# Optimization experiments

Hardware: AMD Instinct MI355X
Metric: run time of the kernel (lower is better)

Reference implementation:

```python
import jax, jax.numpy as jnp
import numpy as np

DN = ('NCHW', 'OIHW', 'NCHW')


def conv2d(x, w, pad, dil):
    return jax.lax.conv_general_dilated(x, w, (1, 1), [(pad, pad), (pad, pad)],
                                        rhs_dilation=(dil, dil), dimension_numbers=DN)


def group_norm(x, scale, bias, groups=16, eps=1e-5):
    B, C, H, W = x.shape
    xg = x.reshape(B, groups, -1)
    mu = xg.mean(-1, keepdims=True)
    var = xg.var(-1, keepdims=True)
    xg = (xg - mu) / jnp.sqrt(var + eps)
    return xg.reshape(B, C, H, W) * scale[None, :, None, None] + bias[None, :, None, None]


def aspp_block(x, w, s, b, pad, dil):
    return jax.nn.relu(group_norm(conv2d(x, w, pad, dil), s, b))


def cc_module(q, k, v):
    # criss-cross attention with channel-cosine-normalized q/k
    eps = 1e-10
    qn = q / (jnp.sqrt(jnp.sum(q * q, axis=1, keepdims=True)) + eps)  # norm over channel
    kn = k / (jnp.sqrt(jnp.sum(k * k, axis=1, keepdims=True)) + eps)
    H = q.shape[2]
    # energy along column (vary h') and row (vary w')
    eH = jnp.einsum('bchw,bcgw->bhwg', qn, kn)  # [B,H,W,H]
    eW = jnp.einsum('bchw,bchv->bhwv', qn, kn)  # [B,H,W,W]
    att = jax.nn.softmax(jnp.concatenate([eH, eW], axis=-1), axis=-1)
    attH, attW = att[..., :H], att[..., H:]
    outH = jnp.einsum('bcgw,bhwg->bchw', v, attH)
    outW = jnp.einsum('bchv,bhwv->bchw', v, attW)
    return outH + outW


def cam_module(x, gamma):
    # channel attention with spatial-cosine-normalized similarity
    B, C, H, W = x.shape
    f = x.reshape(B, C, H * W)
    fn = f / (jnp.sqrt(jnp.sum(f * f, axis=-1, keepdims=True)) + 1e-10)
    energy = jnp.einsum('bcn,bdn->bcd', fn, fn)  # [B,C,C]
    att = jax.nn.softmax(energy, axis=-1)
    out = jnp.einsum('bcd,bdn->bcn', att, f).reshape(B, C, H, W)
    return gamma * out + x


def setup_inputs() -> dict:
    key = jax.random.key(0)
    ks = jax.random.split(key, 32)
    C, Cq = 256, 64
    d = {}
    d['x'] = jax.random.normal(ks[0], (4, C, 128, 128), dtype=jnp.float32)
    d['w1'] = jax.random.normal(ks[1], (C, C, 1, 1), jnp.float32) * 0.05
    d['w2'] = jax.random.normal(ks[2], (C, C, 3, 3), jnp.float32) * 0.02
    d['w3'] = jax.random.normal(ks[3], (C, C, 3, 3), jnp.float32) * 0.02
    d['w4'] = jax.random.normal(ks[4], (C, C, 3, 3), jnp.float32) * 0.02
    d['wc'] = jax.random.normal(ks[5], (C, C, 3, 3), jnp.float32) * 0.02
    for i, nm in enumerate(['s1', 's2', 's3', 's4', 'sc']):
        d[nm] = jnp.ones((C,), jnp.float32)
    for nm in ['b1', 'b2', 'b3', 'b4', 'bc']:
        d[nm] = jnp.zeros((C,), jnp.float32)
    d['wq'] = jax.random.normal(ks[6], (Cq, C, 1, 1), jnp.float32) * 0.05
    d['bq'] = jnp.zeros((Cq,), jnp.float32)
    d['wk'] = jax.random.normal(ks[7], (Cq, C, 1, 1), jnp.float32) * 0.05
    d['bk'] = jnp.zeros((Cq,), jnp.float32)
    d['wv'] = jax.random.normal(ks[8], (C, C, 1, 1), jnp.float32) * 0.05
    d['bv'] = jnp.zeros((C,), jnp.float32)
    d['gammas'] = jax.random.normal(ks[9], (5,), jnp.float32) * 0.1
    return d


def reference(x, w1, w2, w3, w4, wc, s1, s2, s3, s4, sc, b1, b2, b3, b4, bc,
              wq, bq, wk, bk, wv, bv, gammas):
    dil = (1, 6, 12, 18)
    x1 = aspp_block(x, w1, s1, b1, pad=0, dil=dil[0])
    x2 = aspp_block(x, w2, s2, b2, pad=dil[1], dil=dil[1])
    x3 = aspp_block(x, w3, s3, b3, pad=dil[2], dil=dil[2])
    x4 = aspp_block(x, w4, s4, b4, pad=dil[3], dil=dil[3])
    x5 = aspp_block(x, wc, sc, bc, pad=1, dil=1)
    for _ in range(2):
        q = conv2d(x5, wq, 0, 1) + bq[None, :, None, None]
        k = conv2d(x5, wk, 0, 1) + bk[None, :, None, None]
        v = conv2d(x5, wv, 0, 1) + bv[None, :, None, None]
        x5 = cc_module(q, k, v)
    L = [x1, x2, x3, x4, x5]
    L = [cam_module(L[i], gammas[i]) for i in range(5)]
    return jnp.stack(L)  # [5, B, C, H, W]
```

## Files before the change

kernel.cpp:

```cpp
#include <hip/hip_runtime.h>
#include <hip/hip_bf16.h>

typedef __hip_bfloat16 bf16;
typedef unsigned short u16;
typedef __attribute__((ext_vector_type(8))) short short8v;
typedef __attribute__((ext_vector_type(4))) float f32x4;

#define BB   4
#define CC_  256
#define HH   128
#define WW   128
#define HWn  16384
#define SZ   ((size_t)16777216)

__device__ __forceinline__ float b2f(bf16 v){ return __bfloat162float(v); }
__device__ __forceinline__ bf16  f2b(float v){ return __float2bfloat16(v); }
__device__ __forceinline__ float us2f(u16 u){
  union { unsigned int i; float f; } x; x.i = ((unsigned int)u) << 16; return x.f;
}
__device__ __forceinline__ u16 f2us(float v){
  bf16 h = f2b(v); u16 u; __builtin_memcpy(&u, &h, 2); return u;
}
__device__ __forceinline__ void st4(float* p, float a, float b, float c, float d){
  *(float4*)p = make_float4(a,b,c,d);
}
__device__ __forceinline__ void st4(bf16* p, float a, float b, float c, float d){
  bf16 o[4] = { f2b(a), f2b(b), f2b(c), f2b(d) };
  *(uint2*)p = *(uint2*)o;
}
__device__ __forceinline__ void store1(float* p, float v){ *p = v; }
__device__ __forceinline__ void store1(bf16* p, float v){ *p = f2b(v); }

typedef __attribute__((address_space(1))) const unsigned int u32g;
typedef __attribute__((address_space(3))) unsigned int u32l;
__device__ __forceinline__ void gl16(const void* g, void* l)
{
  u32g* gp = (u32g*)(unsigned long long)(size_t)g;
  u32l* lp = (u32l*)(unsigned int)(size_t)l;
  __builtin_amdgcn_global_load_lds(gp, lp, 16, 0, 0);
}

__global__ __launch_bounds__(256)
void k_xpose(const float* __restrict__ x, bf16* __restrict__ xt)
{
  const int b = blockIdx.x >> 7, h = blockIdx.x & 127;
  __shared__ u16 L[64][132];
  const int tid = threadIdx.x;
  for (int c0 = 0; c0 < 256; c0 += 64) {
    for (int idx = tid; idx < 2048; idx += 256) {
      const int c = idx >> 5, w4 = (idx & 31) * 4;
      const float4 v = *(const float4*)&x[(((size_t)(b*CC_ + c0 + c))*HH + h)*WW + w4];
      L[c][w4]   = f2us(v.x); L[c][w4+1] = f2us(v.y);
      L[c][w4+2] = f2us(v.z); L[c][w4+3] = f2us(v.w);
    }
    __syncthreads();
    for (int idx = tid; idx < 1024; idx += 256) {
      const int w = idx >> 3, cg = (idx & 7) * 8;
      u16 tmp[8];
      #pragma unroll
      for (int j = 0; j < 8; ++j) tmp[j] = L[cg + j][w];
      *(uint4*)&xt[(((size_t)(b*HH + h))*WW + w)*256 + c0 + cg] = *(uint4*)tmp;
    }
    __syncthreads();
  }
}

__global__ __launch_bounds__(256)
void k_xposeb_b(const bf16* __restrict__ xt, bf16* __restrict__ fb)
{
  const int b = blockIdx.x >> 7, h = blockIdx.x & 127;
  __shared__ u16 L[64][132];
  const int tid = threadIdx.x;
  for (int c0 = 0; c0 < 256; c0 += 64) {
    for (int idx = tid; idx < 1024; idx += 256) {
      const int w = idx >> 3, cg = (idx & 7) * 8;
      u16 t[8];
      *(uint4*)t = *(const uint4*)((const u16*)xt + (((size_t)(b*HH + h))*WW + w)*256 + c0 + cg);
      #pragma unroll
      for (int j = 0; j < 8; ++j) L[cg + j][w] = t[j];
    }
    __syncthreads();
    for (int idx = tid; idx < 2048; idx += 256) {
      const int c = idx >> 5, w4 = (idx & 31) * 4;
      u16 q[4] = { L[c][w4], L[c][w4+1], L[c][w4+2], L[c][w4+3] };
      *(uint2*)((u16*)fb + (((size_t)(b*CC_ + c0 + c))*HH + h)*WW + w4) = *(uint2*)q;
    }
    __syncthreads();
  }
}

__global__ __launch_bounds__(256)
void k_wt(const float* __restrict__ w, bf16* __restrict__ wt, int taps)
{
  const int i = blockIdx.x * 256 + threadIdx.x;
  const int tap = i >> 16, r = i & 65535;
  const int co = r >> 8, ci = r & 255;
  if (tap < taps) wt[i] = f2b(w[(co*256 + ci)*taps + tap]);
}

template<int KHW, typename DT, bool TRANS, bool STATS>
__global__ __launch_bounds__(256)
void k_convm(const bf16* __restrict__ xt, const bf16* __restrict__ wt,
             const float* __restrict__ bias, DT* __restrict__ dst, int dil, int CO,
             float* __restrict__ stats)
{
  const int b   = blockIdx.y >> 7;
  const int h   = blockIdx.y & 127;
  const int co0 = blockIdx.x * 64;
  const int tid = threadIdx.x;
  const int wid = tid >> 6;
  const int lane = tid & 63;
  const int lr = lane & 15;
  const int lg = lane >> 4;
  const int lrow = lane >> 2;
  const int lci  = (lane & 3) * 8;

  __shared__ __align__(16) u16 Asld[KHW*64][32];
  __shared__ __align__(16) u16 Bsld[164][32];

  for (int i = tid; i < 36*32; i += 256) {
    int r = i >> 5; r = (r < 18) ? r : (128 + r);
    Bsld[r][i & 31] = 0;
  }

  f32x4 acc[4][2] = {};

  for (int kh = 0; kh < KHW; ++kh) {
    const int hh = h + (kh - (KHW >> 1)) * dil;
    if (hh < 0 || hh >= HH) continue;
    const bf16* __restrict__ brow = xt + ((size_t)(b*HH + hh))*WW*256;
    for (int kc = 0; kc < 256; kc += 32) {
      for (int ch = wid; ch < KHW*4; ch += 4) {
        const int row = ch*16 + lrow;
        const int tap = row >> 6, cc = row & 63;
        gl16(wt + ((size_t)(kh*KHW + tap))*CO*256 + (co0 + cc)*256 + kc + lci,
             &Asld[ch*16][0]);
      }
      for (int ch = wid; ch < 8; ch += 4) {
        const int wpos = ch*16 + lrow;
        gl16(brow + (size_t)wpos*256 + kc + lci, &Bsld[18 + ch*16][0]);
      }
      __syncthreads();
      #pragma unroll
      for (int kw = 0; kw < KHW; ++kw) {
        const int pbase = 18 + (kw - (KHW >> 1)) * dil;
        short8v af[4], bfr[2];
        #pragma unroll
        for (int cf = 0; cf < 4; ++cf)
          af[cf] = *(const short8v*)&Asld[kw*64 + cf*16 + lr][lg*8];
        #pragma unroll
        for (int wf = 0; wf < 2; ++wf)
          bfr[wf] = *(const short8v*)&Bsld[pbase + wid*32 + wf*16 + lr][lg*8];
        #pragma unroll
        for (int cf = 0; cf < 4; ++cf)
          #pragma unroll
          for (int wf = 0; wf < 2; ++wf)
            acc[cf][wf] = __builtin_amdgcn_mfma_f32_16x16x32_bf16(
                            af[cf], bfr[wf], acc[cf][wf], 0, 0, 0);
      }
      __syncthreads();
    }
  }
  if constexpr (TRANS) {
    #pragma unroll
    for (int cf = 0; cf < 4; ++cf) {
      float bb[4];
      #pragma unroll
      for (int r = 0; r < 4; ++r)
        bb[r] = bias ? bias[co0 + cf*16 + lg*4 + r] : 0.f;
      #pragma unroll
      for (int wf = 0; wf < 2; ++wf) {
        const int wpix = wid*32 + wf*16 + lr;
        bf16* dr = (bf16*)dst + (((size_t)(b*HH + h))*WW + wpix)*CO + co0 + cf*16 + lg*4;
        bf16 o4[4];
        #pragma unroll
        for (int r = 0; r < 4; ++r) o4[r] = f2b(acc[cf][wf][r] + bb[r]);
        *(uint2*)dr = *(uint2*)o4;
      }
    }
  } else {
    float s0[4] = {0.f,0.f,0.f,0.f}, s1[4] = {0.f,0.f,0.f,0.f};
    #pragma unroll
    for (int cf = 0; cf < 4; ++cf) {
      #pragma unroll
      for (int r = 0; r < 4; ++r) {
        const int co = co0 + cf*16 + lg*4 + r;
        const float bb = bias ? bias[co] : 0.f;
        DT* drow = dst + (((size_t)(b*CO + co))*HH + h)*WW;
        #pragma unroll
        for (int wf = 0; wf < 2; ++wf) {
          const float v = acc[cf][wf][r] + bb;
          store1(drow + wid*32 + wf*16 + lr, v);
          if constexpr (STATS) {
            const float vr = us2f(f2us(v));
            s0[cf] += vr;
            s1[cf] = fmaf(vr, vr, s1[cf]);
          }
        }
      }
    }
    if constexpr (STATS) {
      #pragma unroll
      for (int cf = 0; cf < 4; ++cf)
        #pragma unroll
        for (int o = 32; o > 0; o >>= 1) {
          s0[cf] += __shfl_down(s0[cf], o, 64);
          s1[cf] += __shfl_down(s1[cf], o, 64);
        }
      __shared__ float sred[4][4][2];
      if (lane == 0) {
        #pragma unroll
        for (int cf = 0; cf < 4; ++cf) { sred[wid][cf][0] = s0[cf]; sred[wid][cf][1] = s1[cf]; }
      }
      __syncthreads();
      if (tid < 8) {
        const int cf = tid >> 1, j = tid & 1;
        const float t = sred[0][cf][j] + sred[1][cf][j] + sred[2][cf][j] + sred[3][cf][j];
        atomicAdd(&stats[(b*16 + (co0 >> 4) + cf)*2 + j], t);
      }
    }
  }
}

__global__ __launch_bounds__(256)
void k_gn_apply16(const bf16* __restrict__ t, const float* __restrict__ stats,
                  const float* __restrict__ sc, const float* __restrict__ bi,
                  float* __restrict__ dst)
{
  const size_t e = ((size_t)blockIdx.x * 256 + threadIdx.x) * 4;
  const int c  = (int)((e >> 14) & 255);
  const int bg = (int)(e >> 22) * 16 + (c >> 4);
  const float cnt = 16.f * 16384.f;
  const float mu  = stats[bg*2] / cnt;
  const float var = stats[bg*2+1] / cnt - mu * mu;
  const float rs  = rsqrtf(var + 1e-5f);
  const float a   = rs * sc[c];
  const float bb  = bi[c] - mu * a;
  const ushort4 u = *(const ushort4*)((const u16*)t + e);
  st4(dst + e, fmaxf(us2f(u.x)*a+bb,0.f), fmaxf(us2f(u.y)*a+bb,0.f),
               fmaxf(us2f(u.z)*a+bb,0.f), fmaxf(us2f(u.w)*a+bb,0.f));
}

__global__ __launch_bounds__(256)
void k_gn_applyb(const bf16* __restrict__ t, const float* __restrict__ stats,
                 const float* __restrict__ sc, const float* __restrict__ bi,
                 bf16* __restrict__ dst, float* __restrict__ rownsq)
{
  const size_t e = ((size_t)blockIdx.x * 256 + threadIdx.x) * 4;
  const int c  = (int)((e >> 14) & 255);
  const int bg = (int)(e >> 22) * 16 + (c >> 4);
  const float cnt = 16.f * 16384.f;
  const float mu  = stats[bg*2] / cnt;
  const float var = stats[bg*2+1] / cnt - mu * mu;
  const float rs  = rsqrtf(var + 1e-5f);
  const float a   = rs * sc[c];
  const float bb  = bi[c] - mu * a;
  const ushort4 u = *(const ushort4*)((const u16*)t + e);
  u16 q[4] = { f2us(fmaxf(us2f(u.x)*a+bb,0.f)), f2us(fmaxf(us2f(u.y)*a+bb,0.f)),
               f2us(fmaxf(us2f(u.z)*a+bb,0.f)), f2us(fmaxf(us2f(u.w)*a+bb,0.f)) };
  *(uint2*)((u16*)dst + e) = *(uint2*)q;
  float sq = 0.f;
  #pragma unroll
  for (int j = 0; j < 4; ++j) { const float w = us2f(q[j]); sq = fmaf(w, w, sq); }
  #pragma unroll
  for (int o = 32; o > 0; o >>= 1) sq += __shfl_down(sq, o, 64);
  __shared__ float sh[4];
  const int wid = threadIdx.x >> 6, lane = threadIdx.x & 63;
  if (lane == 0) sh[wid] = sq;
  __syncthreads();
  if (threadIdx.x == 0) atomicAdd(&rownsq[blockIdx.x >> 4], sh[0]+sh[1]+sh[2]+sh[3]);
}

__global__ __launch_bounds__(256)
void k_energym(const bf16* __restrict__ fb, float* __restrict__ energy)
{
  const int b  = blockIdx.z;
  const int c0 = (blockIdx.x >> 1) * 128, d0 = (blockIdx.x & 1) * 128;
  const int k0 = blockIdx.y * 512;
  __shared__ __align__(16) u16 Au[2][128][32];
  __shared__ __align__(16) u16 Bu[2][128][32];
  const int tid = threadIdx.x;
  const int wid = tid >> 6, lane = tid & 63;
  const int lr = lane & 15, lg = lane >> 4;
  const int lrow = lane >> 2, lci = (lane & 3) * 8;
  const int row0w = (wid & 1) * 64, col0w = (wid >> 1) * 64;
  const u16* __restrict__ fbb = (const u16*)fb + (size_t)b * CC_ * HWn;

  f32x4 acc[4][4] = {};

  for (int kc = 0; kc < 512; kc += 64) {
    for (int ci = wid; ci < 16; ci += 4) {
      const int seg = ci >> 3, rq = (ci & 7) * 16;
      const int m = rq + lrow;
      gl16(fbb + (size_t)(c0 + m)*HWn + k0 + kc + seg*32 + lci, &Au[seg][rq][0]);
      gl16(fbb + (size_t)(d0 + m)*HWn + k0 + kc + seg*32 + lci, &Bu[seg][rq][0]);
    }
    __syncthreads();
    #pragma unroll
    for (int ks = 0; ks < 2; ++ks) {
      short8v af[4], bfv[4];
      #pragma unroll
      for (int cf = 0; cf < 4; ++cf)
        af[cf] = *(const short8v*)&Au[ks][row0w + cf*16 + lr][lg*8];
      #pragma unroll
      for (int df = 0; df < 4; ++df)
        bfv[df] = *(const short8v*)&Bu[ks][col0w + df*16 + lr][lg*8];
      #pragma unroll
      for (int cf = 0; cf < 4; ++cf)
        #pragma unroll
        for (int df = 0; df < 4; ++df)
          acc[cf][df] = __builtin_amdgcn_mfma_f32_16x16x32_bf16(
                          af[cf], bfv[df], acc[cf][df], 0, 0, 0);
    }
    __syncthreads();
  }
  #pragma unroll
  for (int cf = 0; cf < 4; ++cf)
    #pragma unroll
    for (int df = 0; df < 4; ++df)
      #pragma unroll
      for (int r = 0; r < 4; ++r) {
        const int row = c0 + row0w + cf*16 + lg*4 + r;
        const int col = d0 + col0w + df*16 + lr;
        atomicAdd(&energy[((size_t)(b*CC_ + row))*CC_ + col], acc[cf][df][r]);
      }
}

__global__ __launch_bounds__(512)
void k_camoutm(const float* __restrict__ catt, const bf16* __restrict__ fb,
               float* __restrict__ fio, const float* __restrict__ gammas, int gi)
{
  const int b  = blockIdx.y;
  const int n0 = blockIdx.x * 128;
  __shared__ u16 Au[256][40];
  __shared__ u16 Bu[128][40];
  const int tid = threadIdx.x;
  const int wid = tid >> 6, lane = tid & 63;
  const int lr = lane & 15, lg = lane >> 4;
  const int row0w = (wid & 3) * 64, col0w = (wid >> 2) * 64;

  f32x4 acc[4][4] = {};

  for (int k0 = 0; k0 < 256; k0 += 32) {
    {
      const int m = tid >> 1, kh = (tid & 1) * 16;
      const float* src = catt + ((size_t)(b*CC_ + m))*CC_ + k0 + kh;
      u16 t[16];
      #pragma unroll
      for (int j = 0; j < 4; ++j) {
        const float4 v = *(const float4*)(src + j*4);
        t[j*4]=f2us(v.x); t[j*4+1]=f2us(v.y); t[j*4+2]=f2us(v.z); t[j*4+3]=f2us(v.w);
      }
      *(uint4*)&Au[m][kh]   = *(uint4*)&t[0];
      *(uint4*)&Au[m][kh+8] = *(uint4*)&t[8];
    }
    {
      const int kk = tid >> 4, cl = tid & 15;
      const u16* src = (const u16*)fb + ((size_t)(b*CC_ + k0 + kk))*HWn + n0 + cl;
      #pragma unroll
      for (int j = 0; j < 8; ++j)
        Bu[cl + 16*j][kk] = src[16*j];
    }
    __syncthreads();
    short8v af[4], bfv[4];
    #pragma unroll
    for (int cf = 0; cf < 4; ++cf)
      af[cf] = *(const short8v*)&Au[row0w + cf*16 + lr][lg*8];
    #pragma unroll
    for (int df = 0; df < 4; ++df)
      bfv[df] = *(const short8v*)&Bu[col0w + df*16 + lr][lg*8];
    #pragma unroll
    for (int cf = 0; cf < 4; ++cf)
      #pragma unroll
      for (int df = 0; df < 4; ++df)
        acc[cf][df] = __builtin_amdgcn_mfma_f32_16x16x32_bf16(
                        af[cf], bfv[df], acc[cf][df], 0, 0, 0);
    __syncthreads();
  }
  const float g = gammas[gi];
  #pragma unroll
  for (int cf = 0; cf < 4; ++cf)
    #pragma unroll
    for (int df = 0; df < 4; ++df)
      #pragma unroll
      for (int r = 0; r < 4; ++r) {
        const int row = row0w + cf*16 + lg*4 + r;
        const int col = n0 + col0w + df*16 + lr;
        const size_t o = ((size_t)(b*CC_ + row))*HWn + col;
        fio[o] = g*acc[cf][df][r] + us2f(((const u16*)fb)[o]);
      }
}

__global__ __launch_bounds__(256)
void k_qknorm_t(bf16* __restrict__ q)
{
  const int pix = blockIdx.x * 256 + threadIdx.x;
  u16* __restrict__ base = (u16*)q + (size_t)pix * 64;
  u16 t[64];
  #pragma unroll
  for (int j = 0; j < 8; ++j) *(uint4*)&t[j*8] = *(const uint4*)(base + j*8);
  float s = 0.f;
  #pragma unroll
  for (int c = 0; c < 64; ++c) { const float v = us2f(t[c]); s = fmaf(v, v, s); }
  const float rn = 1.f / (sqrtf(s) + 1e-10f);
  #pragma unroll
  for (int c = 0; c < 64; ++c) t[c] = f2us(us2f(t[c]) * rn);
  #pragma unroll
  for (int j = 0; j < 8; ++j) *(uint4*)(base + j*8) = *(uint4*)&t[j*8];
}

__global__ __launch_bounds__(256)
void k_attHm(const bf16* __restrict__ qt, const bf16* __restrict__ kt,
             bf16* __restrict__ att)
{
  const int b = blockIdx.x >> 7, w = blockIdx.x & 127;
  __shared__ __align__(16) u16 Qs[2][128][32];
  __shared__ __align__(16) u16 Ks[2][128][32];
  const int tid = threadIdx.x;
  const int wid = tid >> 6, lane = tid & 63;
  const int lr = lane & 15, lg = lane >> 4;
  const int lrow = lane >> 2, lci = (lane & 3) * 8;
  const int h0w = (wid & 1) * 64, g0w = (wid >> 1) * 64;
  for (int ci = wid; ci < 16; ci += 4) {
    const int seg = ci >> 3, rq = (ci & 7) * 16;
    const int row = rq + lrow;
    const size_t gb = (((size_t)(b*HH + row))*WW + w)*64 + seg*32 + lci;
    gl16((const u16*)qt + gb, &Qs[seg][rq][0]);
    gl16((const u16*)kt + gb, &Ks[seg][rq][0]);
  }
  __syncthreads();
  f32x4 acc[4][4] = {};
  #pragma unroll
  for (int ks = 0; ks < 2; ++ks) {
    short8v af[4], bfv[4];
    #pragma unroll
    for (int hf = 0; hf < 4; ++hf)
      af[hf] = *(const short8v*)&Qs[ks][h0w + hf*16 + lr][lg*8];
    #pragma unroll
    for (int gf = 0; gf < 4; ++gf)
      bfv[gf] = *(const short8v*)&Ks[ks][g0w + gf*16 + lr][lg*8];
    #pragma unroll
    for (int hf = 0; hf < 4; ++hf)
      #pragma unroll
      for (int gf = 0; gf < 4; ++gf)
        acc[hf][gf] = __builtin_amdgcn_mfma_f32_16x16x32_bf16(
                        af[hf], bfv[gf], acc[hf][gf], 0, 0, 0);
  }
  #pragma unroll
  for (int hf = 0; hf < 4; ++hf)
    #pragma unroll
    for (int r = 0; r < 4; ++r) {
      const int h = h0w + hf*16 + lg*4 + r;
      u16* prow = (u16*)att + (((size_t)b*HH + h)*WW + w)*256 + g0w;
      #pragma unroll
      for (int gf = 0; gf < 4; ++gf)
        prow[gf*16 + lr] = f2us(acc[hf][gf][r]);
    }
}

__global__ __launch_bounds__(256)
void k_attWm(const bf16* __restrict__ qt, const bf16* __restrict__ kt,
             bf16* __restrict__ att)
{
  const int b = blockIdx.x >> 7, h = blockIdx.x & 127;
  __shared__ __align__(16) u16 Qs[2][128][32];
  __shared__ __align__(16) u16 Ks[2][128][32];
  const int tid = threadIdx.x;
  const int wid = tid >> 6, lane = tid & 63;
  const int lr = lane & 15, lg = lane >> 4;
  const int lrow = lane >> 2, lci = (lane & 3) * 8;
  const int w0w = (wid & 1) * 64, v0w = (wid >> 1) * 64;
  for (int ci = wid; ci < 16; ci += 4) {
    const int seg = ci >> 3, rq = (ci & 7) * 16;
    const int row = rq + lrow;
    const size_t gb = (((size_t)(b*HH + h))*WW + row)*64 + seg*32 + lci;
    gl16((const u16*)qt + gb, &Qs[seg][rq][0]);
    gl16((const u16*)kt + gb, &Ks[seg][rq][0]);
  }
  __syncthreads();
  f32x4 acc[4][4] = {};
  #pragma unroll
  for (int ks = 0; ks < 2; ++ks) {
    short8v af[4], bfv[4];
    #pragma unroll
    for (int wf = 0; wf < 4; ++wf)
      af[wf] = *(const short8v*)&Qs[ks][w0w + wf*16 + lr][lg*8];
    #pragma unroll
    for (int vf = 0; vf < 4; ++vf)
      bfv[vf] = *(const short8v*)&Ks[ks][v0w + vf*16 + lr][lg*8];
    #pragma unroll
    for (int wf = 0; wf < 4; ++wf)
      #pragma unroll
      for (int vf = 0; vf < 4; ++vf)
        acc[wf][vf] = __builtin_amdgcn_mfma_f32_16x16x32_bf16(
                        af[wf], bfv[vf], acc[wf][vf], 0, 0, 0);
  }
  #pragma unroll
  for (int wf = 0; wf < 4; ++wf)
    #pragma unroll
    for (int r = 0; r < 4; ++r) {
      const int wloc = w0w + wf*16 + lg*4 + r;
      u16* prow = (u16*)att + ((((size_t)b*HH + h)*WW + wloc)*256 + 128) + v0w;
      #pragma unroll
      for (int vf = 0; vf < 4; ++vf)
        prow[vf*16 + lr] = f2us(acc[wf][vf][r]);
    }
}

__global__ __launch_bounds__(256)
void k_ccsm(bf16* __restrict__ att)
{
  const int row  = blockIdx.x * 4 + (threadIdx.x >> 6);
  const int lane = threadIdx.x & 63;
  u16* __restrict__ p = (u16*)att + (size_t)row * 256 + lane * 4;
  const ushort4 u = *(const ushort4*)p;
  float v0 = us2f(u.x), v1 = us2f(u.y), v2 = us2f(u.z), v3 = us2f(u.w);
  float m = fmaxf(fmaxf(v0, v1), fmaxf(v2, v3));
  #pragma unroll
  for (int o = 32; o; o >>= 1) m = fmaxf(m, __shfl_xor(m, o, 64));
  const float e0 = __expf(v0-m), e1 = __expf(v1-m), e2 = __expf(v2-m), e3 = __expf(v3-m);
  float s = e0 + e1 + e2 + e3;
  #pragma unroll
  for (int o = 32; o; o >>= 1) s += __shfl_xor(s, o, 64);
  const float inv = 1.f / s;
  st4((bf16*)p, e0*inv, e1*inv, e2*inv, e3*inv);
}

__global__ __launch_bounds__(256)
void k_outWm(const bf16* __restrict__ vt, const bf16* __restrict__ att,
             bf16* __restrict__ yt)
{
  const int b = blockIdx.y >> 7, h = blockIdx.y & 127;
  const int ch0 = blockIdx.x * 128;
  __shared__ u16 As[128][72];
  __shared__ u16 Bs[128][72];
  const int tid = threadIdx.x;
  const int wid = tid >> 6, lane = tid & 63;
  const int lr = lane & 15, lg = lane >> 4;
  const int w0w = (wid & 1) * 64, c0w = (wid >> 1) * 64;

  f32x4 acc[4][4] = {};

  for (int v0 = 0; v0 < 128; v0 += 64) {
    {
      const int row = tid >> 1, kq = (tid & 1) * 32;
      const u16* src = (const u16*)att + ((((size_t)b*HH + h)*WW + row)*256 + 128) + v0 + kq;
      #pragma unroll
      for (int j = 0; j < 4; ++j)
        *(uint4*)&As[row][kq + j*8] = *(const uint4*)(src + j*8);
    }
    {
      const int vv = tid & 63, cg0 = (tid >> 6) * 32;
      #pragma unroll
      for (int j2 = 0; j2 < 4; ++j2) {
        const int c8 = cg0 + j2*8;
        u16 t[8];
        *(uint4*)t = *(const uint4*)((const u16*)vt +
            (((size_t)(b*HH + h))*WW + (v0 + vv))*256 + ch0 + c8);
        #pragma unroll
        for (int jj = 0; jj < 8; ++jj) Bs[c8 + jj][vv] = t[jj];
      }
    }
    __syncthreads();
    #pragma unroll
    for (int ks = 0; ks < 2; ++ks) {
      short8v af[4], bfv[4];
      #pragma unroll
      for (int wf = 0; wf < 4; ++wf)
        af[wf] = *(const short8v*)&As[w0w + wf*16 + lr][ks*32 + lg*8];
      #pragma unroll
      for (int cf = 0; cf < 4; ++cf)
        bfv[cf] = *(const short8v*)&Bs[c0w + cf*16 + lr][ks*32 + lg*8];
      #pragma unroll
      for (int wf = 0; wf < 4; ++wf)
        #pragma unroll
        for (int cf = 0; cf < 4; ++cf)
          acc[wf][cf] = __builtin_amdgcn_mfma_f32_16x16x32_bf16(
                          af[wf], bfv[cf], acc[wf][cf], 0, 0, 0);
    }
    __syncthreads();
  }
  #pragma unroll
  for (int wf = 0; wf < 4; ++wf)
    #pragma unroll
    for (int r = 0; r < 4; ++r) {
      const int wpix = w0w + wf*16 + lg*4 + r;
      u16* drow = (u16*)yt + (((size_t)(b*HH + h))*WW + wpix)*256 + ch0 + c0w;
      #pragma unroll
      for (int cf = 0; cf < 4; ++cf)
        drow[cf*16 + lr] = f2us(acc[wf][cf][r]);
    }
}

__global__ __launch_bounds__(256)
void k_outHm(const bf16* __restrict__ vt, const bf16* __restrict__ att,
             const bf16* __restrict__ yt, bf16* __restrict__ xt)
{
  const int b = blockIdx.y >> 7, w = blockIdx.y & 127;
  const int ch0 = blockIdx.x * 128;
  __shared__ u16 As[128][72];
  __shared__ u16 Bs[128][72];
  const int tid = threadIdx.x;
  const int wid = tid >> 6, lane = tid & 63;
  const int lr = lane & 15, lg = lane >> 4;
  const int h0w = (wid & 1) * 64, c0w = (wid >> 1) * 64;

  f32x4 acc[4][4] = {};

  for (int g0 = 0; g0 < 128; g0 += 64) {
    {
      const int row = tid >> 1, kq = (tid & 1) * 32;
      const u16* src = (const u16*)att + (((size_t)b*HH + row)*WW + w)*256 + g0 + kq;
      #pragma unroll
      for (int j = 0; j < 4; ++j)
        *(uint4*)&As[row][kq + j*8] = *(const uint4*)(src + j*8);
    }
    {
      const int gg = tid & 63, cg0 = (tid >> 6) * 32;
      #pragma unroll
      for (int j2 = 0; j2 < 4; ++j2) {
        const int c8 = cg0 + j2*8;
        u16 t[8];
        *(uint4*)t = *(const uint4*)((const u16*)vt +
            (((size_t)(b*HH + (g0 + gg)))*WW + w)*256 + ch0 + c8);
        #pragma unroll
        for (int jj = 0; jj < 8; ++jj) Bs[c8 + jj][gg] = t[jj];
      }
    }
    __syncthreads();
    #pragma unroll
    for (int ks = 0; ks < 2; ++ks) {
      short8v af[4], bfv[4];
      #pragma unroll
      for (int hf = 0; hf < 4; ++hf)
        af[hf] = *(const short8v*)&As[h0w + hf*16 + lr][ks*32 + lg*8];
      #pragma unroll
      for (int cf = 0; cf < 4; ++cf)
        bfv[cf] = *(const short8v*)&Bs[c0w + cf*16 + lr][ks*32 + lg*8];
      #pragma unroll
      for (int hf = 0; hf < 4; ++hf)
        #pragma unroll
        for (int cf = 0; cf < 4; ++cf)
          acc[hf][cf] = __builtin_amdgcn_mfma_f32_16x16x32_bf16(
                          af[hf], bfv[cf], acc[hf][cf], 0, 0, 0);
    }
    __syncthreads();
  }
  #pragma unroll
  for (int hf = 0; hf < 4; ++hf)
    #pragma unroll
    for (int r = 0; r < 4; ++r) {
      const int hh = h0w + hf*16 + lg*4 + r;
      const size_t base = (((size_t)(b*HH + hh))*WW + w)*256 + ch0 + c0w;
      #pragma unroll
      for (int cf = 0; cf < 4; ++cf) {
        const size_t o = base + cf*16 + lr;
        ((u16*)xt)[o] = f2us(acc[hf][cf][r] + us2f(((const u16*)yt)[o]));
      }
    }
}

__global__ __launch_bounds__(256)
void k_rown16(const bf16* __restrict__ fb, float* __restrict__ rown)
{
  const int bc = blockIdx.x;
  const u16* __restrict__ p = (const u16*)fb + (size_t)bc * HWn;
  float s = 0.f;
  for (int i = threadIdx.x * 8; i < HWn; i += 2048) {
    u16 t[8];
    *(uint4*)t = *(const uint4*)(p + i);
    #pragma unroll
    for (int j = 0; j < 8; ++j) { const float v = us2f(t[j]); s = fmaf(v, v, s); }
  }
  #pragma unroll
  for (int o = 32; o > 0; o >>= 1) s += __shfl_down(s, o, 64);
  __shared__ float sh[4];
  const int wid = threadIdx.x >> 6, lane = threadIdx.x & 63;
  if (lane == 0) sh[wid] = s;
  __syncthreads();
  if (threadIdx.x == 0) rown[bc] = sh[0]+sh[1]+sh[2]+sh[3];
}

__global__ __launch_bounds__(256)
void k_camsm(float* __restrict__ energy, const float* __restrict__ rown)
{
  const int row  = blockIdx.x * 4 + (threadIdx.x >> 6);
  const int lane = threadIdx.x & 63;
  const int b = row >> 8;
  float* __restrict__ p = energy + (size_t)row * 256 + lane * 4;
  const float rc = sqrtf(rown[row]) + 1e-10f;
  float4 rd = *(const float4*)(rown + b*256 + lane*4);
  rd.x = sqrtf(rd.x) + 1e-10f; rd.y = sqrtf(rd.y) + 1e-10f;
  rd.z = sqrtf(rd.z) + 1e-10f; rd.w = sqrtf(rd.w) + 1e-10f;
  float4 v = *(const float4*)p;
  v.x /= (rc*rd.x); v.y /= (rc*rd.y); v.z /= (rc*rd.z); v.w /= (rc*rd.w);
  float m = fmaxf(fmaxf(v.x, v.y), fmaxf(v.z, v.w));
  #pragma unroll
  for (int o = 32; o; o >>= 1) m = fmaxf(m, __shfl_xor(m, o, 64));
  const float e0 = __expf(v.x-m), e1 = __expf(v.y-m), e2 = __expf(v.z-m), e3 = __expf(v.w-m);
  float s = e0 + e1 + e2 + e3;
  #pragma unroll
  for (int o = 32; o; o >>= 1) s += __shfl_xor(s, o, 64);
  const float inv = 1.f / s;
  *(float4*)p = make_float4(e0*inv, e1*inv, e2*inv, e3*inv);
}

extern "C" void kernel_launch(void* const* d_in, const int* in_sizes, int n_in,
                              void* d_out, int out_size, void* d_ws, size_t ws_size,
                              hipStream_t stream)
{
  const float* x     = (const float*)d_in[0];
  const float* w_[5]  = {(const float*)d_in[1],(const float*)d_in[2],(const float*)d_in[3],(const float*)d_in[4],(const float*)d_in[5]};
  const float* s_[5]  = {(const float*)d_in[6],(const float*)d_in[7],(const float*)d_in[8],(const float*)d_in[9],(const float*)d_in[10]};
  const float* bi_[5] = {(const float*)d_in[11],(const float*)d_in[12],(const float*)d_in[13],(const float*)d_in[14],(const float*)d_in[15]};
  const float* wq = (const float*)d_in[16];
  const float* bq = (const float*)d_in[17];
  const float* wk = (const float*)d_in[18];
  const float* bk = (const float*)d_in[19];
  const float* wv = (const float*)d_in[20];
  const float* bv = (const float*)d_in[21];
  const float* gam = (const float*)d_in[22];
  float* out = (float*)d_out;

  char* wsc = (char*)d_ws;
  bf16*  Tc16 = (bf16*)wsc;
  bf16*  qt   = (bf16*)wsc;
  bf16*  kt   = qt + SZ/4;
  bf16*  vt   = qt + SZ/2;
  bf16*  attb = qt + SZ/2 + SZ;
  bf16*  xt   = attb + SZ;
  bf16*  yt   = xt + SZ;
  bf16*  wtb  = yt + SZ;
  bf16*  wtq  = wtb;
  bf16*  wtk  = wtb + 16384;
  bf16*  wtv  = wtb + 32768;
  float* stats  = (float*)(wtb + 16*65536);
  float* energy = stats + 128;
  float* rown   = energy + 262144;
  float* slot4 = out + 4*SZ;
  bf16*  fbA   = attb;
  bf16*  fb16  = vt;

  const int dil_[5] = {1, 6, 12, 18, 1};

  k_xpose<<<512,256,0,stream>>>(x, xt);
  for (int i = 0; i < 4; ++i) {
    hipMemsetAsync(stats, 0, (size_t)(128 + 262144 + 1024)*sizeof(float), stream);
    const int taps = (i == 0) ? 1 : 9;
    k_wt<<<taps*256,256,0,stream>>>(w_[i], wtb, taps);
    if (i == 0) k_convm<1,bf16,false,true><<<dim3(4,512),256,0,stream>>>(xt, wtb, nullptr, Tc16, 1, 256, stats);
    else        k_convm<3,bf16,false,true><<<dim3(4,512),256,0,stream>>>(xt, wtb, nullptr, Tc16, dil_[i], 256, stats);
    k_gn_applyb<<<16384,256,0,stream>>>(Tc16, stats, s_[i], bi_[i], fbA, rown);
    k_energym<<<dim3(4,32,4),256,0,stream>>>(fbA, energy);
    k_camsm<<<256,256,0,stream>>>(energy, rown);
    k_camoutm<<<dim3(128,4),512,0,stream>>>(energy, fbA, out + (size_t)i*SZ, gam, i);
  }

  {
    hipMemsetAsync(stats, 0, 128*sizeof(float), stream);
    k_wt<<<9*256,256,0,stream>>>(w_[4], wtb, 9);
    k_convm<3,bf16,false,true><<<dim3(4,512),256,0,stream>>>(xt, wtb, nullptr, Tc16, 1, 256, stats);
    k_gn_apply16<<<16384,256,0,stream>>>(Tc16, stats, s_[4], bi_[4], slot4);
  }

  k_wt<<<64,256,0,stream>>>(wq, wtq, 1);
  k_wt<<<64,256,0,stream>>>(wk, wtk, 1);
  k_wt<<<256,256,0,stream>>>(wv, wtv, 1);
  k_xpose<<<512,256,0,stream>>>(slot4, xt);
  for (int it = 0; it < 2; ++it) {
    k_convm<1,bf16,true,false><<<dim3(1,512),256,0,stream>>>(xt, wtq, bq, qt, 1, 64, nullptr);
    k_convm<1,bf16,true,false><<<dim3(1,512),256,0,stream>>>(xt, wtk, bk, kt, 1, 64, nullptr);
    k_convm<1,bf16,true,false><<<dim3(4,512),256,0,stream>>>(xt, wtv, bv, vt, 1, 256, nullptr);
    k_qknorm_t<<<256,256,0,stream>>>(qt);
    k_qknorm_t<<<256,256,0,stream>>>(kt);
    k_attHm<<<512,256,0,stream>>>(qt, kt, attb);
    k_attWm<<<512,256,0,stream>>>(qt, kt, attb);
    k_ccsm<<<16384,256,0,stream>>>(attb);
    k_outWm<<<dim3(2,512),256,0,stream>>>(vt, attb, yt);
    k_outHm<<<dim3(2,512),256,0,stream>>>(vt, attb, yt, xt);
  }

  {
    k_xposeb_b<<<512,256,0,stream>>>(xt, fb16);
    hipMemsetAsync(energy, 0, 262144*sizeof(float), stream);
    k_rown16<<<1024,256,0,stream>>>(fb16, rown);
    k_energym<<<dim3(4,32,4),256,0,stream>>>(fb16, energy);
    k_camsm<<<256,256,0,stream>>>(energy, rown);
    k_camoutm<<<dim3(128,4),512,0,stream>>>(energy, fb16, slot4, gam, 4);
  }
}
```

Before: 1.310 ms.

## Fuse GN into transpose, exploit Gram symmetry, fold row norms into transpose

Group-norm for branch 5 is now applied inside the NCHW-to-NHWC transpose, which removes the fp32 write of slot4 and its re-read by a separate transpose. The channel Gram matrix kernel computes only upper-triangular 128x128 blocks (3 of 4) and mirrors off-diagonal results with extra atomics. Row squared norms for the last CAM are accumulated in the transpose-back kernel, which removes the k_rown16 pass. In exchange the energy kernel issues twice the atomics for off-diagonal blocks, and the transpose-back kernel gains per-row atomics.

Result: slower. 1.425 ms (+8.8%).

```diff
diff --git a/kernel.cpp b/kernel.cpp
--- a/kernel.cpp
+++ b/kernel.cpp
@@ -66,7 +66,45 @@
 }
 
 __global__ __launch_bounds__(256)
-void k_xposeb_b(const bf16* __restrict__ xt, bf16* __restrict__ fb)
+void k_xpose_gn(const bf16* __restrict__ t, const float* __restrict__ stats,
+                const float* __restrict__ sc, const float* __restrict__ bi,
+                bf16* __restrict__ xt)
+{
+  const int b = blockIdx.x >> 7, h = blockIdx.x & 127;
+  __shared__ u16 L[64][132];
+  const int tid = threadIdx.x;
+  const float cnt = 16.f * 16384.f;
+  for (int c0 = 0; c0 < 256; c0 += 64) {
+    for (int idx = tid; idx < 1024; idx += 256) {
+      const int c = idx >> 4, w8 = (idx & 15) * 8;
+      const int cg = c0 + c;
+      const int bg = b*16 + (cg >> 4);
+      const float mu  = stats[bg*2] / cnt;
+      const float var = stats[bg*2+1] / cnt - mu * mu;
+      const float a   = rsqrtf(var + 1e-5f) * sc[cg];
+      const float bb  = bi[cg] - mu * a;
+      u16 t8[8];
+      *(uint4*)t8 = *(const uint4*)((const u16*)t + (((size_t)(b*CC_ + cg))*HH + h)*WW + w8);
+      #pragma unroll
+      for (int j = 0; j < 8; ++j) t8[j] = f2us(fmaxf(us2f(t8[j])*a + bb, 0.f));
+      #pragma unroll
+      for (int j = 0; j < 8; ++j) L[c][w8 + j] = t8[j];
+    }
+    __syncthreads();
+    for (int idx = tid; idx < 1024; idx += 256) {
+      const int w = idx >> 3, cg = (idx & 7) * 8;
+      u16 tmp[8];
+      #pragma unroll
+      for (int j = 0; j < 8; ++j) tmp[j] = L[cg + j][w];
+      *(uint4*)&xt[(((size_t)(b*HH + h))*WW + w)*256 + c0 + cg] = *(uint4*)tmp;
+    }
+    __syncthreads();
+  }
+}
+
+__global__ __launch_bounds__(256)
+void k_xposeb_b(const bf16* __restrict__ xt, bf16* __restrict__ fb,
+                float* __restrict__ rownsq)
 {
   const int b = blockIdx.x >> 7, h = blockIdx.x & 127;
   __shared__ u16 L[64][132];
@@ -84,6 +122,12 @@
       const int c = idx >> 5, w4 = (idx & 31) * 4;
       u16 q[4] = { L[c][w4], L[c][w4+1], L[c][w4+2], L[c][w4+3] };
       *(uint2*)((u16*)fb + (((size_t)(b*CC_ + c0 + c))*HH + h)*WW + w4) = *(uint2*)q;
+      float sq = 0.f;
+      #pragma unroll
+      for (int j = 0; j < 4; ++j) { const float v = us2f(q[j]); sq = fmaf(v, v, sq); }
+      #pragma unroll
+      for (int o = 16; o > 0; o >>= 1) sq += __shfl_xor(sq, o, 64);
+      if ((tid & 31) == 0) atomicAdd(&rownsq[b*256 + c0 + c], sq);
     }
     __syncthreads();
   }
@@ -220,25 +264,6 @@
       }
     }
   }
-}
-
-__global__ __launch_bounds__(256)
-void k_gn_apply16(const bf16* __restrict__ t, const float* __restrict__ stats,
-                  const float* __restrict__ sc, const float* __restrict__ bi,
-                  float* __restrict__ dst)
-{
-  const size_t e = ((size_t)blockIdx.x * 256 + threadIdx.x) * 4;
-  const int c  = (int)((e >> 14) & 255);
-  const int bg = (int)(e >> 22) * 16 + (c >> 4);
-  const float cnt = 16.f * 16384.f;
-  const float mu  = stats[bg*2] / cnt;
-  const float var = stats[bg*2+1] / cnt - mu * mu;
-  const float rs  = rsqrtf(var + 1e-5f);
-  const float a   = rs * sc[c];
-  const float bb  = bi[c] - mu * a;
-  const ushort4 u = *(const ushort4*)((const u16*)t + e);
-  st4(dst + e, fmaxf(us2f(u.x)*a+bb,0.f), fmaxf(us2f(u.y)*a+bb,0.f),
-               fmaxf(us2f(u.z)*a+bb,0.f), fmaxf(us2f(u.w)*a+bb,0.f));
 }
 
 __global__ __launch_bounds__(256)
@@ -275,7 +300,8 @@
 void k_energym(const bf16* __restrict__ fb, float* __restrict__ energy)
 {
   const int b  = blockIdx.z;
-  const int c0 = (blockIdx.x >> 1) * 128, d0 = (blockIdx.x & 1) * 128;
+  const int bx = blockIdx.x;
+  const int c0 = (bx >> 1) * 128, d0 = ((bx + 1) >> 1) * 128;
   const int k0 = blockIdx.y * 512;
   __shared__ __align__(16) u16 Au[2][128][32];
   __shared__ __align__(16) u16 Bu[2][128][32];
@@ -314,6 +340,7 @@
     }
     __syncthreads();
   }
+  const bool offd = (c0 != d0);
   #pragma unroll
   for (int cf = 0; cf < 4; ++cf)
     #pragma unroll
@@ -322,7 +349,10 @@
       for (int r = 0; r < 4; ++r) {
         const int row = c0 + row0w + cf*16 + lg*4 + r;
         const int col = d0 + col0w + df*16 + lr;
-        atomicAdd(&energy[((size_t)(b*CC_ + row))*CC_ + col], acc[cf][df][r]);
+        const float v = acc[cf][df][r];
+        atomicAdd(&energy[((size_t)(b*CC_ + row))*CC_ + col], v);
+        if (offd)
+          atomicAdd(&energy[((size_t)(b*CC_ + col))*CC_ + row], v);
       }
 }
 
@@ -658,27 +688,6 @@
         ((u16*)xt)[o] = f2us(acc[hf][cf][r] + us2f(((const u16*)yt)[o]));
       }
     }
-}
-
-__global__ __launch_bounds__(256)
-void k_rown16(const bf16* __restrict__ fb, float* __restrict__ rown)
-{
-  const int bc = blockIdx.x;
-  const u16* __restrict__ p = (const u16*)fb + (size_t)bc * HWn;
-  float s = 0.f;
-  for (int i = threadIdx.x * 8; i < HWn; i += 2048) {
-    u16 t[8];
-    *(uint4*)t = *(const uint4*)(p + i);
-    #pragma unroll
-    for (int j = 0; j < 8; ++j) { const float v = us2f(t[j]); s = fmaf(v, v, s); }
-  }
-  #pragma unroll
-  for (int o = 32; o > 0; o >>= 1) s += __shfl_down(s, o, 64);
-  __shared__ float sh[4];
-  const int wid = threadIdx.x >> 6, lane = threadIdx.x & 63;
-  if (lane == 0) sh[wid] = s;
-  __syncthreads();
-  if (threadIdx.x == 0) rown[bc] = sh[0]+sh[1]+sh[2]+sh[3];
 }
 
 __global__ __launch_bounds__(256)
@@ -751,7 +760,7 @@
     if (i == 0) k_convm<1,bf16,false,true><<<dim3(4,512),256,0,stream>>>(xt, wtb, nullptr, Tc16, 1, 256, stats);
     else        k_convm<3,bf16,false,true><<<dim3(4,512),256,0,stream>>>(xt, wtb, nullptr, Tc16, dil_[i], 256, stats);
     k_gn_applyb<<<16384,256,0,stream>>>(Tc16, stats, s_[i], bi_[i], fbA, rown);
-    k_energym<<<dim3(4,32,4),256,0,stream>>>(fbA, energy);
+    k_energym<<<dim3(3,32,4),256,0,stream>>>(fbA, energy);
     k_camsm<<<256,256,0,stream>>>(energy, rown);
     k_camoutm<<<dim3(128,4),512,0,stream>>>(energy, fbA, out + (size_t)i*SZ, gam, i);
   }
@@ -760,13 +769,12 @@
     hipMemsetAsync(stats, 0, 128*sizeof(float), stream);
     k_wt<<<9*256,256,0,stream>>>(w_[4], wtb, 9);
     k_convm<3,bf16,false,true><<<dim3(4,512),256,0,stream>>>(xt, wtb, nullptr, Tc16, 1, 256, stats);
-    k_gn_apply16<<<16384,256,0,stream>>>(Tc16, stats, s_[4], bi_[4], slot4);
+    k_xpose_gn<<<512,256,0,stream>>>(Tc16, stats, s_[4], bi_[4], xt);
   }
 
   k_wt<<<64,256,0,stream>>>(wq, wtq, 1);
   k_wt<<<64,256,0,stream>>>(wk, wtk, 1);
   k_wt<<<256,256,0,stream>>>(wv, wtv, 1);
-  k_xpose<<<512,256,0,stream>>>(slot4, xt);
   for (int it = 0; it < 2; ++it) {
     k_convm<1,bf16,true,false><<<dim3(1,512),256,0,stream>>>(xt, wtq, bq, qt, 1, 64, nullptr);
     k_convm<1,bf16,true,false><<<dim3(1,512),256,0,stream>>>(xt, wtk, bk, kt, 1, 64, nullptr);
@@ -781,10 +789,9 @@
   }
 
   {
-    k_xposeb_b<<<512,256,0,stream>>>(xt, fb16);
-    hipMemsetAsync(energy, 0, 262144*sizeof(float), stream);
-    k_rown16<<<1024,256,0,stream>>>(fb16, rown);
-    k_energym<<<dim3(4,32,4),256,0,stream>>>(fb16, energy);
+    hipMemsetAsync(energy, 0, (size_t)(262144 + 1024)*sizeof(float), stream);
+    k_xposeb_b<<<512,256,0,stream>>>(xt, fb16, rown);
+    k_energym<<<dim3(3,32,4),256,0,stream>>>(fb16, energy);
     k_camsm<<<256,256,0,stream>>>(energy, rown);
     k_camoutm<<<dim3(128,4),512,0,stream>>>(energy, fb16, slot4, gam, 4);
   }
```
